# Performance work log

Measured on AMD Instinct MI355X. Metric: run time of the kernel, lower is better.

Reference implementation:

```python
import jax, jax.numpy as jnp
import numpy as np

EPS = 1e-5
B, T, D, H = 4096, 256, 36, 64


def setup_inputs() -> dict:
    key = jax.random.key(0)
    ks = jax.random.split(key, 24)
    f32 = jnp.float32
    u = lambda k, shape, s: jax.random.uniform(k, shape, f32, -s, s)
    sH = 1.0 / np.sqrt(H)   # GRUCell / Linear(in=64) init scale
    sD = 1.0 / np.sqrt(D)
    sC = 1.0 / np.sqrt(2 * D)  # combine Linear(72,36)
    return {
        "values": jax.random.normal(ks[0], (B, T, D), f32),
        "masks": (jax.random.uniform(ks[1], (B, T, D)) > 0.2).astype(f32),
        "deltas": jax.random.uniform(ks[2], (B, T, D), f32) * 5.0,
        "label": (jax.random.uniform(ks[3], (B,)) > 0.5).astype(f32),
        "is_train": jnp.ones((B,), f32),
        # GRUCell(108, 64): gate order r, z, n (PyTorch convention)
        "W_ih": u(ks[4], (3 * H, 3 * D), sH),
        "W_hh": u(ks[5], (3 * H, H), sH),
        "b_ih": u(ks[6], (3 * H,), sH),
        "b_hh": u(ks[7], (3 * H,), sH),
        "hist_W": u(ks[8], (1, H), sH),
        "hist_b": u(ks[9], (1,), sH),
        "feat_W": u(ks[10], (D, D), sD),
        "feat_b": u(ks[11], (D,), sD),
        "decay_W": u(ks[12], (D, D), sD),
        "decay_b": u(ks[13], (D,), sD),
        "comb_W": u(ks[14], (D, 2 * D), sC),
        "comb_b": u(ks[15], (D,), sC),
        "out_W": u(ks[16], (1, H), sH),
        "out_b": u(ks[17], (1,), sH),
    }


def reference(values, masks, deltas, label, is_train,
              W_ih, W_hh, b_ih, b_hh, hist_W, hist_b,
              feat_W, feat_b, decay_W, decay_b,
              comb_W, comb_b, out_W, out_b):
    feat_Wm = feat_W * (1.0 - jnp.eye(D, dtype=feat_W.dtype))  # zero diagonal

    def step(carry, xs):
        h, h_sum, il = carry
        value, mask, delta = xs  # each [B, D]
        msum = jnp.sum(mask) + EPS
        value_x = h @ hist_W.T + hist_b                      # [B, 1], broadcasts
        il = il + jnp.sum(jnp.abs(value_x - value) * mask) / msum
        value_c = mask * value + (1.0 - mask) * value_x
        gamma = jnp.exp(-jax.nn.relu(delta @ decay_W.T + decay_b))
        beta = jax.nn.sigmoid(jnp.concatenate([gamma, mask], axis=1) @ comb_W.T + comb_b)
        value_z = value_c @ feat_Wm.T + feat_b
        il = il + jnp.sum(jnp.abs(value_z - value) * mask) / msum
        value_h = value_z * beta + value_x * (1.0 - beta)
        il = il + jnp.sum(jnp.abs(value_h - value) * mask) / msum
        value_c = mask * value + (1.0 - mask) * value_h
        x = jnp.concatenate([value_c, mask, gamma], axis=1)  # [B, 3D]
        gi = x @ W_ih.T + b_ih
        gh = h @ W_hh.T + b_hh
        i_r, i_z, i_n = jnp.split(gi, 3, axis=1)
        h_r, h_z, h_n = jnp.split(gh, 3, axis=1)
        r = jax.nn.sigmoid(i_r + h_r)
        z = jax.nn.sigmoid(i_z + h_z)
        n = jnp.tanh(i_n + r * h_n)
        h_new = (1.0 - z) * n + z * h
        return (h_new, h_sum + h_new, il), value_c

    init = (jnp.zeros((B, H), values.dtype),
            jnp.zeros((B, H), values.dtype),
            jnp.zeros((), values.dtype))
    xs = (values.transpose(1, 0, 2), masks.transpose(1, 0, 2), deltas.transpose(1, 0, 2))
    (h, h_sum, impute_loss), imp = jax.lax.scan(step, init, xs)

    impute_loss = impute_loss / T
    h_sum = h_sum / T
    logits = h_sum @ out_W.T + out_b                          # [B, 1]
    y = label.reshape(-1, 1)
    w = is_train.reshape(-1, 1)
    # binary_cross_entropy_with_logits, reduce=False
    bce = jnp.maximum(logits, 0.0) - logits * y + jnp.log1p(jnp.exp(-jnp.abs(logits)))
    class_loss = jnp.sum(bce * w) / (jnp.sum(w) + EPS)
    loss = class_loss + impute_loss  # alpha = 1.0
    pred = jax.nn.sigmoid(logits)
    impute_values = imp.transpose(1, 0, 2).reshape(B, T * D)  # concat over time on dim 1
    return loss, impute_values, pred
```

## Files before the change

### kernel.cpp

```cpp
#include <hip/hip_runtime.h>
#include <hip/hip_bf16.h>


#define Bsz 4096
#define Tn  256
#define Dn  36
#define ROWS 16
#define EPSf 1e-5f
#define VMST 38

using f32x4 = __attribute__((ext_vector_type(4))) float;
using s8    = __attribute__((ext_vector_type(8))) short;

__device__ __forceinline__ short f2bf(float x) {
  return (short)__bfloat16_as_ushort(__float2bfloat16(x));
}
__device__ __forceinline__ float sigf(float x) { return 1.f / (1.f + __expf(-x)); }
__device__ __forceinline__ float tanhfast(float x) { return 1.f - 2.f / (1.f + __expf(2.f * x)); }
__device__ __forceinline__ int fragoff(int row, int k) {
  return ((k >> 5) << 9) + (((k >> 3) & 3) << 7) + (row << 3) + (k & 7);
}
__device__ __forceinline__ float selq(f32x4 v, int s) {
  float a = (s & 1) ? v[1] : v[0];
  float b = (s & 1) ? v[3] : v[2];
  return (s & 2) ? b : a;
}
#define MFMA __builtin_amdgcn_mfma_f32_16x16x32_bf16

__global__ void msum_k(const float4* __restrict__ masks4, float* __restrict__ rmsum) {
  int t = blockIdx.x;
  float s = 0.f;
  for (int r = threadIdx.x; r < Bsz; r += 256) {
    const float4* mp = masks4 + ((size_t)r * Tn + t) * 9;
    #pragma unroll
    for (int j = 0; j < 9; ++j) { float4 v = mp[j]; s += v.x + v.y + v.z + v.w; }
  }
  __shared__ float red[256];
  red[threadIdx.x] = s;
  __syncthreads();
  for (int k = 128; k > 0; k >>= 1) {
    if (threadIdx.x < k) red[threadIdx.x] += red[threadIdx.x + k];
    __syncthreads();
  }
  if (threadIdx.x == 0) rmsum[t] = 1.f / (red[0] + EPSf);
}

__global__ __launch_bounds__(512) void brits_main(
    const float* __restrict__ values, const float* __restrict__ masks,
    const float* __restrict__ deltas, const float* __restrict__ label,
    const float* __restrict__ is_train,
    const float* __restrict__ W_ih, const float* __restrict__ W_hh,
    const float* __restrict__ b_ih, const float* __restrict__ b_hh,
    const float* __restrict__ hist_W, const float* __restrict__ hist_b,
    const float* __restrict__ feat_W, const float* __restrict__ feat_b,
    const float* __restrict__ decay_W, const float* __restrict__ decay_b,
    const float* __restrict__ comb_W, const float* __restrict__ comb_b,
    const float* __restrict__ out_W, const float* __restrict__ out_b,
    float* __restrict__ out, const float* __restrict__ rmsum,
    float* __restrict__ ws_acc ) {

  __shared__ __align__(16) float2 vm_s[2][ROWS * VMST];
  __shared__ __align__(16) short hbuf[1024];
  __shared__ __align__(16) short dbuf[2][1024];
  __shared__ __align__(16) short xbuf[2][2048];
  __shared__ __align__(16) short vcbuf[4][1024];
  __shared__ float red_s[512];
  __shared__ float red16[16];

  const int tid  = threadIdx.x;
  const int w    = tid >> 6;
  const int lane = tid & 63;
  const int lc   = lane & 15;
  const int r4   = lane >> 4;
  const int row0 = blockIdx.x * ROWS;
  const int k0b  = r4 * 8;
  const int lw8  = lane * 8;

  const bool isG = (w < 4);
  const int  sW  = isG ? 0 : (w - 4);
  const int  dim = 16 * (isG ? w : 0) + lc;
  const int  myrow = 4 * r4 + sW;

  s8 bf[23];
  #pragma unroll
  for (int i = 0; i < 23; ++i) bf[i] = (s8)(short)0;

  if (isG) {
    #pragma unroll
    for (int g = 0; g < 3; ++g) {
      const int n = 64 * g + dim;
      #pragma unroll
      for (int kt = 0; kt < 4; ++kt) {
        s8 f;
        #pragma unroll
        for (int e = 0; e < 8; ++e) {
          int xk = k0b + 32 * kt + e;
          float wv = 0.f;
          if (xk < 72) wv = W_ih[n * 108 + 36 + xk];
          else if (xk < 108) wv = W_ih[n * 108 + xk - 72];
          f[e] = f2bf(wv);
        }
        bf[g * 4 + kt] = f;
      }
      #pragma unroll
      for (int kt = 0; kt < 2; ++kt) {
        s8 f;
        #pragma unroll
        for (int e = 0; e < 8; ++e) f[e] = f2bf(W_hh[n * 64 + k0b + 32 * kt + e]);
        bf[12 + g * 2 + kt] = f;
      }
    }
  } else {
    #pragma unroll
    for (int t3 = 0; t3 < 3; ++t3) {
      const int col = 16 * t3 + lc;
      const bool cok = (col < Dn);
      #pragma unroll
      for (int kt = 0; kt < 2; ++kt) {
        s8 fd, ff;
        #pragma unroll
        for (int e = 0; e < 8; ++e) {
          int k = k0b + 32 * kt + e;
          fd[e] = f2bf((cok && k < Dn) ? decay_W[col * Dn + k] : 0.f);
          ff[e] = f2bf((cok && k < Dn && k != col) ? feat_W[col * Dn + k] : 0.f);
        }
        bf[t3 * 2 + kt] = fd;
        bf[6 + t3 * 2 + kt] = ff;
      }
      #pragma unroll
      for (int kt = 0; kt < 3; ++kt) {
        s8 f;
        #pragma unroll
        for (int e = 0; e < 8; ++e) {
          int xk = k0b + 32 * kt + e;
          float wv = 0.f;
          if (cok) {
            if (xk < 36) wv = comb_W[col * 72 + 36 + xk];
            else if (xk < 72) wv = comb_W[col * 72 + xk - 36];
          }
          f[e] = f2bf(wv);
        }
        bf[14 + t3 * 3 + kt] = f;
      }
    }
    #pragma unroll
    for (int kt = 0; kt < 2; ++kt) {
      s8 f;
      #pragma unroll
      for (int e = 0; e < 8; ++e) f[e] = f2bf(hist_W[k0b + 32 * kt + e]);
      bf[12 + kt] = f;
    }
  }

  float db3[3] = {0,0,0}, fb3[3] = {0,0,0}, cb3[3] = {0,0,0};
  float br = 0.f, bz = 0.f, bin_ = 0.f, bhn = 0.f, ow = 0.f;
  if (isG) {
    br   = b_ih[dim] + b_hh[dim];
    bz   = b_ih[64 + dim] + b_hh[64 + dim];
    bin_ = b_ih[128 + dim];
    bhn  = b_hh[128 + dim];
    ow   = out_W[dim];
  } else {
    #pragma unroll
    for (int t3 = 0; t3 < 3; ++t3) {
      int col = 16 * t3 + lc;
      if (col < Dn) { db3[t3] = decay_b[col]; fb3[t3] = feat_b[col]; cb3[t3] = comb_b[col]; }
    }
  }
  const float histb = hist_b[0];
  const int hb = fragoff(0, dim);

  const bool stg = (tid < 144);
  const int srow = tid / 9;
  const int squad = tid - srow * 9;
  const size_t sbase = ((size_t)(row0 + srow) * Tn) * Dn + squad * 4;
  const int sfo = fragoff(srow, squad * 4);
  const int svo = srow * VMST + squad * 4;

  for (int i = tid; i < 1024; i += 512) {
    hbuf[i] = 0; dbuf[0][i] = 0; dbuf[1][i] = 0;
    vcbuf[0][i] = 0; vcbuf[1][i] = 0; vcbuf[2][i] = 0; vcbuf[3][i] = 0;
  }
  for (int i = tid; i < 2048; i += 512) { xbuf[0][i] = 0; xbuf[1][i] = 0; }
  __syncthreads();

  float4 pv = {0,0,0,0}, pm = {0,0,0,0}, pd = {0,0,0,0};
  if (stg) {
    float4 v0 = *(const float4*)&values[sbase];
    float4 m0 = *(const float4*)&masks[sbase];
    float4 d0 = *(const float4*)&deltas[sbase];
    *(float4*)&vm_s[0][svo]     = make_float4(v0.x, m0.x, v0.y, m0.y);
    *(float4*)&vm_s[0][svo + 2] = make_float4(v0.z, m0.z, v0.w, m0.w);
    union { short s[4]; uint2 u; } td, tm;
    td.s[0]=f2bf(d0.x); td.s[1]=f2bf(d0.y); td.s[2]=f2bf(d0.z); td.s[3]=f2bf(d0.w);
    tm.s[0]=f2bf(m0.x); tm.s[1]=f2bf(m0.y); tm.s[2]=f2bf(m0.z); tm.s[3]=f2bf(m0.w);
    *(uint2*)&dbuf[0][sfo] = td.u;
    *(uint2*)&xbuf[0][sfo] = tm.u;
    pv = *(const float4*)&values[sbase + Dn];
    pm = *(const float4*)&masks[sbase + Dn];
    pd = *(const float4*)&deltas[sbase + Dn];
  }
  __syncthreads();

  float bq[3] = {0.f, 0.f, 0.f};
  if (!isG) {
    s8 ad0 = *(const s8*)&dbuf[0][lw8];
    s8 ad1 = *(const s8*)&dbuf[0][512 + lw8];
    f32x4 G0 = {0,0,0,0}, G1 = {0,0,0,0}, G2 = {0,0,0,0};
    G0 = MFMA(ad0, bf[0], G0, 0,0,0); G0 = MFMA(ad1, bf[1], G0, 0,0,0);
    G1 = MFMA(ad0, bf[2], G1, 0,0,0); G1 = MFMA(ad1, bf[3], G1, 0,0,0);
    G2 = MFMA(ad0, bf[4], G2, 0,0,0); G2 = MFMA(ad1, bf[5], G2, 0,0,0);
    #pragma unroll
    for (int t3 = 0; t3 < 3; ++t3) {
      int col = 16 * t3 + lc;
      if (col < Dn) {
        float gm = (t3==0) ? selq(G0,sW) : (t3==1) ? selq(G1,sW) : selq(G2,sW);
        xbuf[0][fragoff(myrow, 36 + col)] = f2bf(__expf(-fmaxf(gm + db3[t3], 0.f)));
      }
    }
    s8 ac0 = *(const s8*)&xbuf[0][lw8];
    s8 ac1 = *(const s8*)&xbuf[0][512 + lw8];
    s8 ac2 = *(const s8*)&xbuf[0][1024 + lw8];
    f32x4 B0 = {0,0,0,0}, B1 = {0,0,0,0}, B2 = {0,0,0,0};
    B0 = MFMA(ac0, bf[14], B0, 0,0,0); B0 = MFMA(ac1, bf[15], B0, 0,0,0);
    B0 = MFMA(ac2, bf[16], B0, 0,0,0);
    B1 = MFMA(ac0, bf[17], B1, 0,0,0); B1 = MFMA(ac1, bf[18], B1, 0,0,0);
    B1 = MFMA(ac2, bf[19], B1, 0,0,0);
    B2 = MFMA(ac0, bf[20], B2, 0,0,0); B2 = MFMA(ac1, bf[21], B2, 0,0,0);
    B2 = MFMA(ac2, bf[22], B2, 0,0,0);
    bq[0] = sigf(selq(B0,sW) + cb3[0]);
    bq[1] = sigf(selq(B1,sW) + cb3[1]);
    bq[2] = sigf(selq(B2,sW) + cb3[2]);
  }

  float hreg[4] = {0.f, 0.f, 0.f, 0.f};
  float lacc[4] = {0.f, 0.f, 0.f, 0.f};
  float il = 0.f;
  __syncthreads();

  #pragma unroll 2
  for (int t = 0; t < Tn; ++t) {
    const float srm = rmsum[t];
    const int p = t & 1;
    short* __restrict__ xb  = xbuf[p];
    short* __restrict__ xb2 = xbuf[p ^ 1];
    short* __restrict__ db2 = dbuf[p ^ 1];
    f32x4 A0 = {0,0,0,0}, A1 = {0,0,0,0}, A2 = {0,0,0,0}, A3 = {0,0,0,0};

    if (isG) {
      s8 ah0 = *(const s8*)&hbuf[lw8];
      s8 ah1 = *(const s8*)&hbuf[512 + lw8];
      A0 = MFMA(ah0, bf[12], A0, 0,0,0); A0 = MFMA(ah1, bf[13], A0, 0,0,0);
      A1 = MFMA(ah0, bf[14], A1, 0,0,0); A1 = MFMA(ah1, bf[15], A1, 0,0,0);
      A3 = MFMA(ah0, bf[16], A3, 0,0,0); A3 = MFMA(ah1, bf[17], A3, 0,0,0);
      s8 ax0 = *(const s8*)&xb[lw8];
      s8 ax1 = *(const s8*)&xb[512 + lw8];
      A0 = MFMA(ax0, bf[0], A0, 0,0,0); A0 = MFMA(ax1, bf[1], A0, 0,0,0);
      A1 = MFMA(ax0, bf[4], A1, 0,0,0); A1 = MFMA(ax1, bf[5], A1, 0,0,0);
      A2 = MFMA(ax0, bf[8], A2, 0,0,0); A2 = MFMA(ax1, bf[9], A2, 0,0,0);
      if (stg && t + 1 < Tn) {
        *(float4*)&vm_s[p ^ 1][svo]     = make_float4(pv.x, pm.x, pv.y, pm.y);
        *(float4*)&vm_s[p ^ 1][svo + 2] = make_float4(pv.z, pm.z, pv.w, pm.w);
        union { short s[4]; uint2 u; } td, tm;
        td.s[0]=f2bf(pd.x); td.s[1]=f2bf(pd.y); td.s[2]=f2bf(pd.z); td.s[3]=f2bf(pd.w);
        tm.s[0]=f2bf(pm.x); tm.s[1]=f2bf(pm.y); tm.s[2]=f2bf(pm.z); tm.s[3]=f2bf(pm.w);
        *(uint2*)&db2[sfo] = td.u;
        *(uint2*)&xb2[sfo] = tm.u;
      }
      if (stg && t + 2 < Tn) {
        size_t o = sbase + (size_t)(t + 2) * Dn;
        pv = *(const float4*)&values[o];
        pm = *(const float4*)&masks[o];
        pd = *(const float4*)&deltas[o];
      }
    } else {
      s8 ah0 = *(const s8*)&hbuf[lw8];
      s8 ah1 = *(const s8*)&hbuf[512 + lw8];
      f32x4 X = {0,0,0,0};
      X = MFMA(ah0, bf[12], X, 0,0,0);
      X = MFMA(ah1, bf[13], X, 0,0,0);
      const float vx = selq(X, sW) + histb;
      float v3[3], m3[3];
      #pragma unroll
      for (int t3 = 0; t3 < 3; ++t3) {
        int col = 16 * t3 + lc;
        v3[t3] = 0.f; m3[t3] = 0.f;
        if (col < Dn) {
          float2 vm = vm_s[p][myrow * VMST + col];
          v3[t3] = vm.x; m3[t3] = vm.y;
          il += srm * fabsf(vx - vm.x) * vm.y;
          vcbuf[sW][fragoff(myrow, col)] = f2bf(vm.y * vm.x + (1.f - vm.y) * vx);
        }
      }
      s8 av0 = *(const s8*)&vcbuf[sW][lw8];
      s8 av1 = *(const s8*)&vcbuf[sW][512 + lw8];
      f32x4 Z0 = {0,0,0,0}, Z1 = {0,0,0,0}, Z2 = {0,0,0,0};
      Z0 = MFMA(av0, bf[6],  Z0, 0,0,0); Z0 = MFMA(av1, bf[7],  Z0, 0,0,0);
      Z1 = MFMA(av0, bf[8],  Z1, 0,0,0); Z1 = MFMA(av1, bf[9],  Z1, 0,0,0);
      Z2 = MFMA(av0, bf[10], Z2, 0,0,0); Z2 = MFMA(av1, bf[11], Z2, 0,0,0);
      #pragma unroll
      for (int t3 = 0; t3 < 3; ++t3) {
        int col = 16 * t3 + lc;
        if (col < Dn) {
          float vz = ((t3==0) ? selq(Z0,sW) : (t3==1) ? selq(Z1,sW) : selq(Z2,sW)) + fb3[t3];
          il += srm * fabsf(vz - v3[t3]) * m3[t3];
          float vh = vz * bq[t3] + vx * (1.f - bq[t3]);
          il += srm * fabsf(vh - v3[t3]) * m3[t3];
          float vc2 = m3[t3] * v3[t3] + (1.f - m3[t3]) * vh;
          out[1 + ((size_t)(row0 + myrow) * Tn + t) * Dn + col] = vc2;
          xb[fragoff(myrow, 72 + col)] = f2bf(vc2);
        }
      }
    }
    __syncthreads();

    if (isG) {
      s8 ax2 = *(const s8*)&xb[1024 + lw8];
      s8 ax3 = *(const s8*)&xb[1536 + lw8];
      A0 = MFMA(ax2, bf[2],  A0, 0,0,0); A0 = MFMA(ax3, bf[3],  A0, 0,0,0);
      A1 = MFMA(ax2, bf[6],  A1, 0,0,0); A1 = MFMA(ax3, bf[7],  A1, 0,0,0);
      A2 = MFMA(ax2, bf[10], A2, 0,0,0); A2 = MFMA(ax3, bf[11], A2, 0,0,0);
      #pragma unroll
      for (int q = 0; q < 4; ++q) {
        float rg = sigf(A0[q] + br);
        float zg = sigf(A1[q] + bz);
        float ng = tanhfast(A2[q] + bin_ + rg * (A3[q] + bhn));
        float hn = (1.f - zg) * ng + zg * hreg[q];
        hreg[q] = hn;
        lacc[q] += hn * ow;
        hbuf[hb + (r4 * 4 + q) * 8] = f2bf(hn);
      }
    } else if (t + 1 < Tn) {
      s8 ad0 = *(const s8*)&db2[lw8];
      s8 ad1 = *(const s8*)&db2[512 + lw8];
      f32x4 G0 = {0,0,0,0}, G1 = {0,0,0,0}, G2 = {0,0,0,0};
      G0 = MFMA(ad0, bf[0], G0, 0,0,0); G0 = MFMA(ad1, bf[1], G0, 0,0,0);
      G1 = MFMA(ad0, bf[2], G1, 0,0,0); G1 = MFMA(ad1, bf[3], G1, 0,0,0);
      G2 = MFMA(ad0, bf[4], G2, 0,0,0); G2 = MFMA(ad1, bf[5], G2, 0,0,0);
      #pragma unroll
      for (int t3 = 0; t3 < 3; ++t3) {
        int col = 16 * t3 + lc;
        if (col < Dn) {
          float gm = (t3==0) ? selq(G0,sW) : (t3==1) ? selq(G1,sW) : selq(G2,sW);
          xb2[fragoff(myrow, 36 + col)] = f2bf(__expf(-fmaxf(gm + db3[t3], 0.f)));
        }
      }
      s8 ac0 = *(const s8*)&xb2[lw8];
      s8 ac1 = *(const s8*)&xb2[512 + lw8];
      s8 ac2 = *(const s8*)&xb2[1024 + lw8];
      f32x4 B0 = {0,0,0,0}, B1 = {0,0,0,0}, B2 = {0,0,0,0};
      B0 = MFMA(ac0, bf[14], B0, 0,0,0); B0 = MFMA(ac1, bf[15], B0, 0,0,0);
      B0 = MFMA(ac2, bf[16], B0, 0,0,0);
      B1 = MFMA(ac0, bf[17], B1, 0,0,0); B1 = MFMA(ac1, bf[18], B1, 0,0,0);
      B1 = MFMA(ac2, bf[19], B1, 0,0,0);
      B2 = MFMA(ac0, bf[20], B2, 0,0,0); B2 = MFMA(ac1, bf[21], B2, 0,0,0);
      B2 = MFMA(ac2, bf[22], B2, 0,0,0);
      bq[0] = sigf(selq(B0,sW) + cb3[0]);
      bq[1] = sigf(selq(B1,sW) + cb3[1]);
      bq[2] = sigf(selq(B2,sW) + cb3[2]);
    }
    __syncthreads();
  }

  red_s[tid] = il;
  __syncthreads();
  for (int k = 256; k > 0; k >>= 1) {
    if (tid < k) red_s[tid] += red_s[tid + k];
    __syncthreads();
  }
  if (tid == 0) atomicAdd(&ws_acc[0], red_s[0]);
  if (tid < 16) red16[tid] = 0.f;
  __syncthreads();
  if (isG) {
    #pragma unroll
    for (int q = 0; q < 4; ++q) atomicAdd(&red16[r4 * 4 + q], lacc[q]);
  }
  __syncthreads();

  if (tid < ROWS) {
    float lg = red16[tid] / (float)Tn + out_b[0];
    int rg = row0 + tid;
    float pred = sigf(lg);
    out[1 + (size_t)Bsz * Tn * Dn + rg] = pred;
    float y = label[rg], wt = is_train[rg];
    float bce = fmaxf(lg, 0.f) - lg * y + log1pf(__expf(-fabsf(lg)));
    atomicAdd(&ws_acc[1], bce * wt);
    atomicAdd(&ws_acc[2], wt);
  }
}

__global__ void fin_k(const float* __restrict__ ws, float* __restrict__ out) {
  out[0] = ws[1] / (ws[2] + EPSf) + ws[0] / (float)Tn;
}

extern "C" void kernel_launch(void* const* d_in, const int* in_sizes, int n_in,
                              void* d_out, int out_size, void* d_ws, size_t ws_size,
                              hipStream_t stream) {
  const float* values   = (const float*)d_in[0];
  const float* masks    = (const float*)d_in[1];
  const float* deltas   = (const float*)d_in[2];
  const float* label    = (const float*)d_in[3];
  const float* is_train = (const float*)d_in[4];
  const float* W_ih     = (const float*)d_in[5];
  const float* W_hh     = (const float*)d_in[6];
  const float* b_ih     = (const float*)d_in[7];
  const float* b_hh     = (const float*)d_in[8];
  const float* hist_W   = (const float*)d_in[9];
  const float* hist_b   = (const float*)d_in[10];
  const float* feat_W   = (const float*)d_in[11];
  const float* feat_b   = (const float*)d_in[12];
  const float* decay_W  = (const float*)d_in[13];
  const float* decay_b  = (const float*)d_in[14];
  const float* comb_W   = (const float*)d_in[15];
  const float* comb_b   = (const float*)d_in[16];
  const float* out_W    = (const float*)d_in[17];
  const float* out_b    = (const float*)d_in[18];

  float* ws = (float*)d_ws;
  float* rmsum = ws + 4;
  float* out = (float*)d_out;

  hipMemsetAsync(d_ws, 0, 16, stream);
  msum_k<<<Tn, 256, 0, stream>>>((const float4*)masks, rmsum);
  brits_main<<<Bsz / ROWS, 512, 0, stream>>>(
      values, masks, deltas, label, is_train, W_ih, W_hh, b_ih, b_hh,
      hist_W, hist_b, feat_W, feat_b, decay_W, decay_b, comb_W, comb_b,
      out_W, out_b, out, rmsum, ws);
  fin_k<<<1, 1, 0, stream>>>(ws, out);
}
```

Before: 458.3 us.

## Decompose feature regression by linearity to precompute mask terms off the critical path

Because value_c = m*v + (1-m)*vx with scalar vx, value_z can be written as vx*(rowsum(Wm) - Wm·m) + Wm·(m*v) + b. The two mask-dependent products are now computed one step ahead in the non-GRU waves, alongside the decay/beta MFMAs. The per-step vcbuf write, the barrier-free LDS round trip and six MFMAs on the sequential path are replaced by a few FMAs. The cost is an extra mvbuf staging buffer and more MFMAs in the prefetch phase. It also changes rounding: m*v is now rounded to bf16 where m*v + (1-m)*vx was rounded before.

```diff
diff --git a/kernel.cpp b/kernel.cpp
--- a/kernel.cpp
+++ b/kernel.cpp
@@ -62,8 +62,8 @@
   __shared__ __align__(16) float2 vm_s[2][ROWS * VMST];
   __shared__ __align__(16) short hbuf[1024];
   __shared__ __align__(16) short dbuf[2][1024];
+  __shared__ __align__(16) short mvbuf[2][1024];
   __shared__ __align__(16) short xbuf[2][2048];
-  __shared__ __align__(16) short vcbuf[4][1024];
   __shared__ float red_s[512];
   __shared__ float red16[16];
 
@@ -152,7 +152,7 @@
     }
   }
 
-  float db3[3] = {0,0,0}, fb3[3] = {0,0,0}, cb3[3] = {0,0,0};
+  float db3[3] = {0,0,0}, fb3[3] = {0,0,0}, cb3[3] = {0,0,0}, wfs3[3] = {0,0,0};
   float br = 0.f, bz = 0.f, bin_ = 0.f, bhn = 0.f, ow = 0.f;
   if (isG) {
     br   = b_ih[dim] + b_hh[dim];
@@ -164,7 +164,12 @@
     #pragma unroll
     for (int t3 = 0; t3 < 3; ++t3) {
       int col = 16 * t3 + lc;
-      if (col < Dn) { db3[t3] = decay_b[col]; fb3[t3] = feat_b[col]; cb3[t3] = comb_b[col]; }
+      if (col < Dn) {
+        db3[t3] = decay_b[col]; fb3[t3] = feat_b[col]; cb3[t3] = comb_b[col];
+        float s = 0.f;
+        for (int k = 0; k < Dn; ++k) if (k != col) s += feat_W[col * Dn + k];
+        wfs3[t3] = s;
+      }
     }
   }
   const float histb = hist_b[0];
@@ -179,7 +184,7 @@
 
   for (int i = tid; i < 1024; i += 512) {
     hbuf[i] = 0; dbuf[0][i] = 0; dbuf[1][i] = 0;
-    vcbuf[0][i] = 0; vcbuf[1][i] = 0; vcbuf[2][i] = 0; vcbuf[3][i] = 0;
+    mvbuf[0][i] = 0; mvbuf[1][i] = 0;
   }
   for (int i = tid; i < 2048; i += 512) { xbuf[0][i] = 0; xbuf[1][i] = 0; }
   __syncthreads();
@@ -191,25 +196,40 @@
     float4 d0 = *(const float4*)&deltas[sbase];
     *(float4*)&vm_s[0][svo]     = make_float4(v0.x, m0.x, v0.y, m0.y);
     *(float4*)&vm_s[0][svo + 2] = make_float4(v0.z, m0.z, v0.w, m0.w);
-    union { short s[4]; uint2 u; } td, tm;
+    union { short s[4]; uint2 u; } td, tm, tv;
     td.s[0]=f2bf(d0.x); td.s[1]=f2bf(d0.y); td.s[2]=f2bf(d0.z); td.s[3]=f2bf(d0.w);
     tm.s[0]=f2bf(m0.x); tm.s[1]=f2bf(m0.y); tm.s[2]=f2bf(m0.z); tm.s[3]=f2bf(m0.w);
+    tv.s[0]=f2bf(m0.x*v0.x); tv.s[1]=f2bf(m0.y*v0.y);
+    tv.s[2]=f2bf(m0.z*v0.z); tv.s[3]=f2bf(m0.w*v0.w);
     *(uint2*)&dbuf[0][sfo] = td.u;
     *(uint2*)&xbuf[0][sfo] = tm.u;
+    *(uint2*)&mvbuf[0][sfo] = tv.u;
     pv = *(const float4*)&values[sbase + Dn];
     pm = *(const float4*)&masks[sbase + Dn];
     pd = *(const float4*)&deltas[sbase + Dn];
   }
   __syncthreads();
 
-  float bq[3] = {0.f, 0.f, 0.f};
+  float bq[3] = {0,0,0}, mvv[3] = {0,0,0}, msv[3] = {0,0,0};
   if (!isG) {
     s8 ad0 = *(const s8*)&dbuf[0][lw8];
     s8 ad1 = *(const s8*)&dbuf[0][512 + lw8];
-    f32x4 G0 = {0,0,0,0}, G1 = {0,0,0,0}, G2 = {0,0,0,0};
+    s8 am0 = *(const s8*)&xbuf[0][lw8];
+    s8 am1 = *(const s8*)&xbuf[0][512 + lw8];
+    s8 av0 = *(const s8*)&mvbuf[0][lw8];
+    s8 av1 = *(const s8*)&mvbuf[0][512 + lw8];
+    f32x4 G0={0,0,0,0}, G1={0,0,0,0}, G2={0,0,0,0};
+    f32x4 S0={0,0,0,0}, S1={0,0,0,0}, S2={0,0,0,0};
+    f32x4 V0={0,0,0,0}, V1={0,0,0,0}, V2={0,0,0,0};
     G0 = MFMA(ad0, bf[0], G0, 0,0,0); G0 = MFMA(ad1, bf[1], G0, 0,0,0);
     G1 = MFMA(ad0, bf[2], G1, 0,0,0); G1 = MFMA(ad1, bf[3], G1, 0,0,0);
     G2 = MFMA(ad0, bf[4], G2, 0,0,0); G2 = MFMA(ad1, bf[5], G2, 0,0,0);
+    S0 = MFMA(am0, bf[6], S0, 0,0,0); S0 = MFMA(am1, bf[7], S0, 0,0,0);
+    S1 = MFMA(am0, bf[8], S1, 0,0,0); S1 = MFMA(am1, bf[9], S1, 0,0,0);
+    S2 = MFMA(am0, bf[10], S2, 0,0,0); S2 = MFMA(am1, bf[11], S2, 0,0,0);
+    V0 = MFMA(av0, bf[6], V0, 0,0,0); V0 = MFMA(av1, bf[7], V0, 0,0,0);
+    V1 = MFMA(av0, bf[8], V1, 0,0,0); V1 = MFMA(av1, bf[9], V1, 0,0,0);
+    V2 = MFMA(av0, bf[10], V2, 0,0,0); V2 = MFMA(av1, bf[11], V2, 0,0,0);
     #pragma unroll
     for (int t3 = 0; t3 < 3; ++t3) {
       int col = 16 * t3 + lc;
@@ -217,16 +237,17 @@
         float gm = (t3==0) ? selq(G0,sW) : (t3==1) ? selq(G1,sW) : selq(G2,sW);
         xbuf[0][fragoff(myrow, 36 + col)] = f2bf(__expf(-fmaxf(gm + db3[t3], 0.f)));
       }
-    }
-    s8 ac0 = *(const s8*)&xbuf[0][lw8];
+      msv[t3] = (t3==0) ? selq(S0,sW) : (t3==1) ? selq(S1,sW) : selq(S2,sW);
+      mvv[t3] = (t3==0) ? selq(V0,sW) : (t3==1) ? selq(V1,sW) : selq(V2,sW);
+    }
     s8 ac1 = *(const s8*)&xbuf[0][512 + lw8];
     s8 ac2 = *(const s8*)&xbuf[0][1024 + lw8];
-    f32x4 B0 = {0,0,0,0}, B1 = {0,0,0,0}, B2 = {0,0,0,0};
-    B0 = MFMA(ac0, bf[14], B0, 0,0,0); B0 = MFMA(ac1, bf[15], B0, 0,0,0);
+    f32x4 B0={0,0,0,0}, B1={0,0,0,0}, B2={0,0,0,0};
+    B0 = MFMA(am0, bf[14], B0, 0,0,0); B0 = MFMA(ac1, bf[15], B0, 0,0,0);
     B0 = MFMA(ac2, bf[16], B0, 0,0,0);
-    B1 = MFMA(ac0, bf[17], B1, 0,0,0); B1 = MFMA(ac1, bf[18], B1, 0,0,0);
+    B1 = MFMA(am0, bf[17], B1, 0,0,0); B1 = MFMA(ac1, bf[18], B1, 0,0,0);
     B1 = MFMA(ac2, bf[19], B1, 0,0,0);
-    B2 = MFMA(ac0, bf[20], B2, 0,0,0); B2 = MFMA(ac1, bf[21], B2, 0,0,0);
+    B2 = MFMA(am0, bf[20], B2, 0,0,0); B2 = MFMA(ac1, bf[21], B2, 0,0,0);
     B2 = MFMA(ac2, bf[22], B2, 0,0,0);
     bq[0] = sigf(selq(B0,sW) + cb3[0]);
     bq[1] = sigf(selq(B1,sW) + cb3[1]);
@@ -245,6 +266,7 @@
     short* __restrict__ xb  = xbuf[p];
     short* __restrict__ xb2 = xbuf[p ^ 1];
     short* __restrict__ db2 = dbuf[p ^ 1];
+    short* __restrict__ mv2 = mvbuf[p ^ 1];
     f32x4 A0 = {0,0,0,0}, A1 = {0,0,0,0}, A2 = {0,0,0,0}, A3 = {0,0,0,0};
 
     if (isG) {
@@ -261,11 +283,14 @@
       if (stg && t + 1 < Tn) {
         *(float4*)&vm_s[p ^ 1][svo]     = make_float4(pv.x, pm.x, pv.y, pm.y);
         *(float4*)&vm_s[p ^ 1][svo + 2] = make_float4(pv.z, pm.z, pv.w, pm.w);
-        union { short s[4]; uint2 u; } td, tm;
+        union { short s[4]; uint2 u; } td, tm, tv;
         td.s[0]=f2bf(pd.x); td.s[1]=f2bf(pd.y); td.s[2]=f2bf(pd.z); td.s[3]=f2bf(pd.w);
         tm.s[0]=f2bf(pm.x); tm.s[1]=f2bf(pm.y); tm.s[2]=f2bf(pm.z); tm.s[3]=f2bf(pm.w);
+        tv.s[0]=f2bf(pm.x*pv.x); tv.s[1]=f2bf(pm.y*pv.y);
+        tv.s[2]=f2bf(pm.z*pv.z); tv.s[3]=f2bf(pm.w*pv.w);
         *(uint2*)&db2[sfo] = td.u;
         *(uint2*)&xb2[sfo] = tm.u;
+        *(uint2*)&mv2[sfo] = tv.u;
       }
       if (stg && t + 2 < Tn) {
         size_t o = sbase + (size_t)(t + 2) * Dn;
@@ -280,33 +305,16 @@
       X = MFMA(ah0, bf[12], X, 0,0,0);
       X = MFMA(ah1, bf[13], X, 0,0,0);
       const float vx = selq(X, sW) + histb;
-      float v3[3], m3[3];
-      #pragma unroll
-      for (int t3 = 0; t3 < 3; ++t3) {
-        int col = 16 * t3 + lc;
-        v3[t3] = 0.f; m3[t3] = 0.f;
-        if (col < Dn) {
-          float2 vm = vm_s[p][myrow * VMST + col];
-          v3[t3] = vm.x; m3[t3] = vm.y;
-          il += srm * fabsf(vx - vm.x) * vm.y;
-          vcbuf[sW][fragoff(myrow, col)] = f2bf(vm.y * vm.x + (1.f - vm.y) * vx);
-        }
-      }
-      s8 av0 = *(const s8*)&vcbuf[sW][lw8];
-      s8 av1 = *(const s8*)&vcbuf[sW][512 + lw8];
-      f32x4 Z0 = {0,0,0,0}, Z1 = {0,0,0,0}, Z2 = {0,0,0,0};
-      Z0 = MFMA(av0, bf[6],  Z0, 0,0,0); Z0 = MFMA(av1, bf[7],  Z0, 0,0,0);
-      Z1 = MFMA(av0, bf[8],  Z1, 0,0,0); Z1 = MFMA(av1, bf[9],  Z1, 0,0,0);
-      Z2 = MFMA(av0, bf[10], Z2, 0,0,0); Z2 = MFMA(av1, bf[11], Z2, 0,0,0);
       #pragma unroll
       for (int t3 = 0; t3 < 3; ++t3) {
         int col = 16 * t3 + lc;
         if (col < Dn) {
-          float vz = ((t3==0) ? selq(Z0,sW) : (t3==1) ? selq(Z1,sW) : selq(Z2,sW)) + fb3[t3];
-          il += srm * fabsf(vz - v3[t3]) * m3[t3];
+          float2 vm = vm_s[p][myrow * VMST + col];
+          float vz = vx * (wfs3[t3] - msv[t3]) + mvv[t3] + fb3[t3];
           float vh = vz * bq[t3] + vx * (1.f - bq[t3]);
-          il += srm * fabsf(vh - v3[t3]) * m3[t3];
-          float vc2 = m3[t3] * v3[t3] + (1.f - m3[t3]) * vh;
+          float vc2 = vm.y * vm.x + (1.f - vm.y) * vh;
+          il += srm * vm.y *
+                (fabsf(vx - vm.x) + fabsf(vz - vm.x) + fabsf(vh - vm.x));
           out[1 + ((size_t)(row0 + myrow) * Tn + t) * Dn + col] = vc2;
           xb[fragoff(myrow, 72 + col)] = f2bf(vc2);
         }
@@ -333,10 +341,22 @@
     } else if (t + 1 < Tn) {
       s8 ad0 = *(const s8*)&db2[lw8];
       s8 ad1 = *(const s8*)&db2[512 + lw8];
-      f32x4 G0 = {0,0,0,0}, G1 = {0,0,0,0}, G2 = {0,0,0,0};
+      s8 am0 = *(const s8*)&xb2[lw8];
+      s8 am1 = *(const s8*)&xb2[512 + lw8];
+      s8 av0 = *(const s8*)&mv2[lw8];
+      s8 av1 = *(const s8*)&mv2[512 + lw8];
+      f32x4 G0={0,0,0,0}, G1={0,0,0,0}, G2={0,0,0,0};
+      f32x4 S0={0,0,0,0}, S1={0,0,0,0}, S2={0,0,0,0};
+      f32x4 V0={0,0,0,0}, V1={0,0,0,0}, V2={0,0,0,0};
       G0 = MFMA(ad0, bf[0], G0, 0,0,0); G0 = MFMA(ad1, bf[1], G0, 0,0,0);
       G1 = MFMA(ad0, bf[2], G1, 0,0,0); G1 = MFMA(ad1, bf[3], G1, 0,0,0);
       G2 = MFMA(ad0, bf[4], G2, 0,0,0); G2 = MFMA(ad1, bf[5], G2, 0,0,0);
+      S0 = MFMA(am0, bf[6], S0, 0,0,0); S0 = MFMA(am1, bf[7], S0, 0,0,0);
+      S1 = MFMA(am0, bf[8], S1, 0,0,0); S1 = MFMA(am1, bf[9], S1, 0,0,0);
+      S2 = MFMA(am0, bf[10], S2, 0,0,0); S2 = MFMA(am1, bf[11], S2, 0,0,0);
+      V0 = MFMA(av0, bf[6], V0, 0,0,0); V0 = MFMA(av1, bf[7], V0, 0,0,0);
+      V1 = MFMA(av0, bf[8], V1, 0,0,0); V1 = MFMA(av1, bf[9], V1, 0,0,0);
+      V2 = MFMA(av0, bf[10], V2, 0,0,0); V2 = MFMA(av1, bf[11], V2, 0,0,0);
       #pragma unroll
       for (int t3 = 0; t3 < 3; ++t3) {
         int col = 16 * t3 + lc;
@@ -344,16 +364,17 @@
           float gm = (t3==0) ? selq(G0,sW) : (t3==1) ? selq(G1,sW) : selq(G2,sW);
           xb2[fragoff(myrow, 36 + col)] = f2bf(__expf(-fmaxf(gm + db3[t3], 0.f)));
         }
-      }
-      s8 ac0 = *(const s8*)&xb2[lw8];
+        msv[t3] = (t3==0) ? selq(S0,sW) : (t3==1) ? selq(S1,sW) : selq(S2,sW);
+        mvv[t3] = (t3==0) ? selq(V0,sW) : (t3==1) ? selq(V1,sW) : selq(V2,sW);
+      }
       s8 ac1 = *(const s8*)&xb2[512 + lw8];
       s8 ac2 = *(const s8*)&xb2[1024 + lw8];
-      f32x4 B0 = {0,0,0,0}, B1 = {0,0,0,0}, B2 = {0,0,0,0};
-      B0 = MFMA(ac0, bf[14], B0, 0,0,0); B0 = MFMA(ac1, bf[15], B0, 0,0,0);
+      f32x4 B0={0,0,0,0}, B1={0,0,0,0}, B2={0,0,0,0};
+      B0 = MFMA(am0, bf[14], B0, 0,0,0); B0 = MFMA(ac1, bf[15], B0, 0,0,0);
       B0 = MFMA(ac2, bf[16], B0, 0,0,0);
-      B1 = MFMA(ac0, bf[17], B1, 0,0,0); B1 = MFMA(ac1, bf[18], B1, 0,0,0);
+      B1 = MFMA(am0, bf[17], B1, 0,0,0); B1 = MFMA(ac1, bf[18], B1, 0,0,0);
       B1 = MFMA(ac2, bf[19], B1, 0,0,0);
-      B2 = MFMA(ac0, bf[20], B2, 0,0,0); B2 = MFMA(ac1, bf[21], B2, 0,0,0);
+      B2 = MFMA(am0, bf[20], B2, 0,0,0); B2 = MFMA(ac1, bf[21], B2, 0,0,0);
       B2 = MFMA(ac2, bf[22], B2, 0,0,0);
       bq[0] = sigf(selq(B0,sW) + cb3[0]);
       bq[1] = sigf(selq(B1,sW) + cb3[1]);
```

Measured after the change: 426.2 us. 7.0% less time.
